# Kernel tuning notes

Hardware: AMD Instinct MI355X
Metric: run time of the kernel (lower is better)

## Reference

```python
import jax, jax.numpy as jnp
import numpy as np

WIDTH = 1024
NUM_HEADS = 16
HEAD_DIM = WIDTH // NUM_HEADS  # 64
WINDOW = 256
BATCH = 2
SEQ = 2048
_MIN_LOGITS_VALUE = -1e30


def setup_inputs() -> dict:
    key = jax.random.key(0)
    ks = jax.random.split(key, 6)
    std = 1.0 / np.sqrt(WIDTH)
    x = jax.random.normal(ks[0], (BATCH, SEQ, WIDTH), dtype=jnp.float32)
    Wq = jax.random.normal(ks[1], (WIDTH, WIDTH), dtype=jnp.float32) * std
    Wk = jax.random.normal(ks[2], (HEAD_DIM, WIDTH), dtype=jnp.float32) * std
    Wv = jax.random.normal(ks[3], (HEAD_DIM, WIDTH), dtype=jnp.float32) * std
    Wf = jax.random.normal(ks[4], (WIDTH, WIDTH), dtype=jnp.float32) * std  # variance_scale=1.0
    bf = jnp.zeros((WIDTH,), dtype=jnp.float32)
    return {"x": x, "Wq": Wq, "Wk": Wk, "Wv": Wv, "Wf": Wf, "bf": bf}


def reference(x, Wq, Wk, Wv, Wf, bf):
    b, t, _ = x.shape
    # projections (torch Linear: y = x @ W.T)
    q = (x @ Wq.T).reshape(b, t, NUM_HEADS, HEAD_DIM)  # b t n h
    k = x @ Wk.T  # b t h  (MQA: single shared key head)
    v = x @ Wv.T  # b t h
    scale = 1.0 / np.sqrt(HEAD_DIM)
    # logits: queries per-head against the shared key head
    logits = jnp.einsum('btnh,bsh->bnts', q, k) * scale  # b n t s
    # symmetric local window mask |i - j| <= WINDOW
    pos = jnp.arange(t)
    mask = jnp.abs(pos[:, None] - pos[None, :]) <= WINDOW  # t s
    masked = jnp.where(mask[None, None, :, :], logits, _MIN_LOGITS_VALUE)
    probs = jax.nn.softmax(masked.astype(jnp.float32), axis=-1).astype(logits.dtype)
    out = jnp.einsum('bnts,bsh->btnh', probs, v).reshape(b, t, WIDTH)
    return out @ Wf.T + bf
```

## Files before the change

kernel.cpp:

```cpp
#include <hip/hip_runtime.h>

typedef __bf16 bf16;
typedef __bf16 bf16x8 __attribute__((ext_vector_type(8)));
typedef float  f32x4  __attribute__((ext_vector_type(4)));

#define MFMA(a, b, c) __builtin_amdgcn_mfma_f32_16x16x32_bf16((a), (b), (c), 0, 0, 0)

static constexpr int B_   = 2;
static constexpr int T_   = 2048;
static constexpr int D_   = 1024;
static constexpr int NH_  = 16;
static constexpr int HD_  = 64;
static constexpr int WIN_ = 256;
static constexpr int M_   = B_ * T_;
static constexpr int NQKV = D_ + 2 * HD_;

static constexpr float QSCALE = 0.125f * 1.44269504088896f;

__device__ __forceinline__ void gld_lds16(const bf16* g, bf16* l) {
  __builtin_amdgcn_global_load_lds(
      (const __attribute__((address_space(1))) void*)g,
      (__attribute__((address_space(3))) void*)l, 16, 0, 0);
}


__global__ __launch_bounds__(256) void conv_all(
    const float* __restrict__ x,  const float* __restrict__ wq,
    const float* __restrict__ wk, const float* __restrict__ wv,
    const float* __restrict__ wf, const float* __restrict__ bv,
    bf16* __restrict__ xc, bf16* __restrict__ wqkv,
    bf16* __restrict__ wfc, bf16* __restrict__ bfc) {
  const long i = (long)(blockIdx.x * 256 + threadIdx.x) * 4;
  const float* src; bf16* dst; long off;
  if      (i < 4194304L) { src = x;  dst = xc;              off = 0; }
  else if (i < 5242880L) { src = wq; dst = wqkv;            off = 4194304L; }
  else if (i < 5308416L) { src = wk; dst = wqkv + 1048576L; off = 5242880L; }
  else if (i < 5373952L) { src = wv; dst = wqkv + 1114112L; off = 5308416L; }
  else if (i < 6422528L) { src = wf; dst = wfc;             off = 5373952L; }
  else if (i < 6423552L) { src = bv; dst = bfc;             off = 6422528L; }
  else return;
  const long j = i - off;
  const float4 v = *(const float4*)(src + j);
  bf16 o[4] = {(bf16)v.x, (bf16)v.y, (bf16)v.z, (bf16)v.w};
  *(uint2*)(dst + j) = *(const uint2*)o;
}

template <int EPI>
__global__ __launch_bounds__(256) void gemm128x128(
    const bf16* __restrict__ A, const bf16* __restrict__ Bw,
    void* __restrict__ Cout, const bf16* __restrict__ bias,
    bf16* __restrict__ kb, bf16* __restrict__ vT, int N, int K) {
  __shared__ __align__(16) bf16 As[2][128 * 64];
  __shared__ __align__(16) bf16 Bs[2][128 * 64];

  const int tid  = threadIdx.x;
  const int w    = tid >> 6;
  const int lane = tid & 63;
  const int quad = lane >> 4;
  const int l16  = lane & 15;
  const int wm   = w & 1;
  const int wn   = w >> 1;
  const int m0   = blockIdx.x * 128;
  const int n0   = blockIdx.y * 128;
  const int lrow = lane >> 3;
  const int scol = ((lane & 7) ^ lrow) * 8;
  const int rx   = (l16 & 7) * 8;

  f32x4 acc[4][4] = {};

  auto stage = [&](int buf, int k0) {
#pragma unroll
    for (int t = 0; t < 8; ++t) {
      const int inst = w * 8 + t;
      if (inst < 16) {
        gld_lds16(&A[(size_t)(m0 + inst * 8 + lrow) * K + k0 + scol],
                  &As[buf][inst * 512]);
      } else {
        const int bi = inst - 16;
        gld_lds16(&Bw[(size_t)(n0 + bi * 8 + lrow) * K + k0 + scol],
                  &Bs[buf][bi * 512]);
      }
    }
  };

  auto compute = [&](int buf) {
#pragma unroll
    for (int kk = 0; kk < 64; kk += 32) {
      const int c = (kk + quad * 8) ^ rx;
      bf16x8 a[4], b[4];
#pragma unroll
      for (int i = 0; i < 4; ++i)
        a[i] = *(const bf16x8*)&As[buf][(wm * 64 + i * 16 + l16) * 64 + c];
#pragma unroll
      for (int j = 0; j < 4; ++j)
        b[j] = *(const bf16x8*)&Bs[buf][(wn * 64 + j * 16 + l16) * 64 + c];
#pragma unroll
      for (int i = 0; i < 4; ++i)
#pragma unroll
        for (int j = 0; j < 4; ++j) acc[i][j] = MFMA(a[i], b[j], acc[i][j]);
    }
  };

  stage(0, 0);
  __syncthreads();
  int cur = 0;
  for (int k0 = 64; k0 < K; k0 += 64) {
    stage(cur ^ 1, k0);
    compute(cur);
    __syncthreads();
    cur ^= 1;
  }
  compute(cur);

#pragma unroll
  for (int i = 0; i < 4; ++i) {
#pragma unroll
    for (int j = 0; j < 4; ++j) {
      const int col     = n0 + wn * 64 + j * 16 + l16;
      const int rowbase = m0 + wm * 64 + i * 16 + quad * 4;
      if (EPI == 1) {
        if (col < D_) {
          bf16* qb = (bf16*)Cout;
#pragma unroll
          for (int r = 0; r < 4; ++r)
            qb[(size_t)(rowbase + r) * D_ + col] = (bf16)(acc[i][j][r] * QSCALE);
        } else if (col < D_ + HD_) {
#pragma unroll
          for (int r = 0; r < 4; ++r)
            kb[(size_t)(rowbase + r) * HD_ + (col - D_)] = (bf16)acc[i][j][r];
        } else {
          bf16 o[4] = {(bf16)acc[i][j][0], (bf16)acc[i][j][1],
                       (bf16)acc[i][j][2], (bf16)acc[i][j][3]};
          *(uint2*)&vT[(size_t)(col - D_ - HD_) * M_ + rowbase] = *(const uint2*)o;
        }
      } else {
        float* outp = (float*)Cout;
        const float bvv = (float)bias[col];
#pragma unroll
        for (int r = 0; r < 4; ++r)
          outp[(size_t)(rowbase + r) * D_ + col] = acc[i][j][r] + bvv;
      }
    }
  }
}

__global__ __launch_bounds__(256) void attn_win128(
    const bf16* __restrict__ q, const bf16* __restrict__ k,
    const bf16* __restrict__ vT, bf16* __restrict__ o) {
  __shared__ __align__(16) bf16 Ks[2][64 * 64];
  __shared__ __align__(16) bf16 Vt[2][64 * 64];
  __shared__ __align__(16) bf16 Ps[128 * 72];
  __shared__ float ls[4][32];

  const int tid  = threadIdx.x;
  const int w    = tid >> 6;
  const int lane = tid & 63;
  const int quad = lane >> 4;
  const int l16  = lane & 15;
  const int lrow = lane >> 3;
  const int scol = ((lane & 7) ^ lrow) * 8;
  const int rx   = (l16 & 7) * 8;

  const int t0 = blockIdx.x * 128;
  const int n  = blockIdx.y;
  const int b  = blockIdx.z;

  auto stageKV = [&](int st, int pb) {
#pragma unroll
    for (int t = 0; t < 2; ++t) {
      const int inst = w * 2 + t;
      gld_lds16(&k[((size_t)(b * T_ + st + inst * 8 + lrow)) * HD_ + scol],
                &Ks[pb][inst * 512]);
      gld_lds16(&vT[(size_t)(inst * 8 + lrow) * M_ + b * T_ + st + scol],
                &Vt[pb][inst * 512]);
    }
  };

  const int st_lo = (t0 - WIN_ > 0) ? t0 - WIN_ : 0;
  const int st_hi = (t0 + WIN_ + 64 < T_ - 64) ? t0 + WIN_ + 64 : T_ - 64;

  stageKV(st_lo, 0);
  int pb = 0;

  bf16x8 qf[2][2];
#pragma unroll
  for (int tt = 0; tt < 2; ++tt)
#pragma unroll
    for (int kq = 0; kq < 2; ++kq)
      qf[tt][kq] = *(const bf16x8*)
          &q[((size_t)(b * T_ + t0 + w * 32 + tt * 16 + l16)) * D_ +
             n * HD_ + kq * 32 + quad * 8];

  f32x4 o_acc[2][4] = {};
  float l_part[2] = {0.0f, 0.0f};

  for (int st = st_lo; st <= st_hi; st += 64) {
    __syncthreads();
    if (st + 64 <= st_hi) stageKV(st + 64, pb ^ 1);

    f32x4 sacc[4][2] = {};
#pragma unroll
    for (int kk = 0; kk < 64; kk += 32) {
      const int c = (kk + quad * 8) ^ rx;
      bf16x8 ak[4];
#pragma unroll
      for (int stile = 0; stile < 4; ++stile)
        ak[stile] = *(const bf16x8*)&Ks[pb][(stile * 16 + l16) * 64 + c];
      __builtin_amdgcn_s_setprio(1);
#pragma unroll
      for (int stile = 0; stile < 4; ++stile)
#pragma unroll
        for (int tt = 0; tt < 2; ++tt)
          sacc[stile][tt] = MFMA(ak[stile], qf[tt][kk >> 5], sacc[stile][tt]);
      __builtin_amdgcn_s_setprio(0);
    }

    const int off_t = st - t0;
    const bool need_mask =
        (off_t < w * 32 - (WIN_ - 31)) || (off_t > w * 32 + (WIN_ - 63));
    if (!need_mask) {
#pragma unroll
      for (int tt = 0; tt < 2; ++tt) {
#pragma unroll
        for (int stile = 0; stile < 4; ++stile) {
          bf16 pk[4];
          float psum = 0.0f;
#pragma unroll
          for (int r = 0; r < 4; ++r) {
            const float p =
                __builtin_amdgcn_exp2f(fminf(sacc[stile][tt][r], 43.28f));
            psum += p;
            pk[r] = (bf16)p;
          }
          l_part[tt] += psum;
          *(uint2*)&Ps[(w * 32 + tt * 16 + l16) * 72 + stile * 16 + quad * 4] =
              *(const uint2*)pk;
        }
      }
    } else {
#pragma unroll
      for (int tt = 0; tt < 2; ++tt) {
        const int t   = t0 + w * 32 + tt * 16 + l16;
        const int tlo = t0 + w * 32 + tt * 16;
#pragma unroll
        for (int stile = 0; stile < 4; ++stile) {
          const int slo = st + stile * 16;
          if (slo - (tlo + 15) > WIN_ || tlo - (slo + 15) > WIN_) {
            const uint2 z = {0u, 0u};
            *(uint2*)&Ps[(w * 32 + tt * 16 + l16) * 72 + stile * 16 + quad * 4] = z;
          } else {
            bf16 pk[4];
            float psum = 0.0f;
#pragma unroll
            for (int r = 0; r < 4; ++r) {
              const int s = slo + quad * 4 + r;
              const int d = t - s;
              const float p =
                  (d > WIN_ || d < -WIN_)
                      ? 0.0f
                      : __builtin_amdgcn_exp2f(fminf(sacc[stile][tt][r], 43.28f));
              psum += p;
              pk[r] = (bf16)p;
            }
            l_part[tt] += psum;
            *(uint2*)&Ps[(w * 32 + tt * 16 + l16) * 72 + stile * 16 + quad * 4] =
                *(const uint2*)pk;
          }
        }
      }
    }

#pragma unroll
    for (int kk = 0; kk < 64; kk += 32) {
      const int c = (kk + quad * 8) ^ rx;
      bf16x8 ap[2];
#pragma unroll
      for (int rg = 0; rg < 2; ++rg)
        ap[rg] = *(const bf16x8*)&Ps[(w * 32 + rg * 16 + l16) * 72 + kk + quad * 8];
      __builtin_amdgcn_s_setprio(1);
#pragma unroll
      for (int nt = 0; nt < 4; ++nt) {
        bf16x8 bv = *(const bf16x8*)&Vt[pb][(nt * 16 + l16) * 64 + c];
#pragma unroll
        for (int rg = 0; rg < 2; ++rg)
          o_acc[rg][nt] = MFMA(ap[rg], bv, o_acc[rg][nt]);
      }
      __builtin_amdgcn_s_setprio(0);
    }
    pb ^= 1;
  }

#pragma unroll
  for (int tt = 0; tt < 2; ++tt) {
    l_part[tt] += __shfl_xor(l_part[tt], 16);
    l_part[tt] += __shfl_xor(l_part[tt], 32);
    if (quad == 0) ls[w][tt * 16 + l16] = l_part[tt];
  }
  __syncthreads();

#pragma unroll
  for (int rg = 0; rg < 2; ++rg) {
#pragma unroll
    for (int r = 0; r < 4; ++r) {
      const float lr = ls[w][rg * 16 + quad * 4 + r] + 1e-30f;
      const int t = t0 + w * 32 + rg * 16 + quad * 4 + r;
#pragma unroll
      for (int nt = 0; nt < 4; ++nt) {
        const int h = nt * 16 + l16;
        o[((size_t)(b * T_ + t)) * D_ + n * HD_ + h] =
            (bf16)(o_acc[rg][nt][r] / lr);
      }
    }
  }
}

extern "C" void kernel_launch(void* const* d_in, const int* in_sizes, int n_in,
                              void* d_out, int out_size, void* d_ws, size_t ws_size,
                              hipStream_t stream) {
  float* out = (float*)d_out;

  bf16* xc   = (bf16*)d_ws;
  bf16* wqkv = xc   + (size_t)M_ * D_;
  bf16* wfc  = wqkv + (size_t)NQKV * D_;
  bf16* bfc  = wfc  + (size_t)D_ * D_;
  bf16* qb   = bfc  + D_;
  bf16* kb   = qb   + (size_t)M_ * D_;
  bf16* vT   = kb   + (size_t)M_ * HD_;

  dim3 blk(256);
  conv_all<<<dim3((6423552 / 4 + 255) / 256), blk, 0, stream>>>(
      (const float*)d_in[0], (const float*)d_in[1], (const float*)d_in[2],
      (const float*)d_in[3], (const float*)d_in[4], (const float*)d_in[5],
      xc, wqkv, wfc, bfc);

  gemm128x128<1><<<dim3(M_ / 128, NQKV / 128), blk, 0, stream>>>(
      xc, wqkv, (void*)qb, nullptr, kb, vT, NQKV, D_);

  attn_win128<<<dim3(T_ / 128, NH_, B_), blk, 0, stream>>>(qb, kb, vT, qb);

  gemm128x128<2><<<dim3(M_ / 128, D_ / 128), blk, 0, stream>>>(
      qb, wfc, (void*)out, bfc, nullptr, nullptr, D_, D_);
}
```

Baseline: 138.9 us.

## Skip out-of-window KV steps per wave and compute row sums via MFMA

Each wave now checks whether the current 64-key step lies entirely outside the window for its 32 query rows and skips the QK, softmax and PV work for that step. The softmax denominator is no longer summed in fp32 with shuffles and an LDS reduction; it comes from an extra MFMA of the bf16 probabilities against a ones vector, which also removes the final __syncthreads. The trade-off is that the row sum is now taken from bf16-rounded probabilities, and waves in a block may diverge in how much work they do between barriers.

```diff
diff --git a/kernel.cpp b/kernel.cpp
--- a/kernel.cpp
+++ b/kernel.cpp
@@ -150,7 +150,6 @@
   __shared__ __align__(16) bf16 Ks[2][64 * 64];
   __shared__ __align__(16) bf16 Vt[2][64 * 64];
   __shared__ __align__(16) bf16 Ps[128 * 72];
-  __shared__ float ls[4][32];
 
   const int tid  = threadIdx.x;
   const int w    = tid >> 6;
@@ -164,6 +163,7 @@
   const int t0 = blockIdx.x * 128;
   const int n  = blockIdx.y;
   const int b  = blockIdx.z;
+  const int tw = t0 + w * 32;
 
   auto stageKV = [&](int st, int pb) {
 #pragma unroll
@@ -188,122 +188,115 @@
 #pragma unroll
     for (int kq = 0; kq < 2; ++kq)
       qf[tt][kq] = *(const bf16x8*)
-          &q[((size_t)(b * T_ + t0 + w * 32 + tt * 16 + l16)) * D_ +
+          &q[((size_t)(b * T_ + tw + tt * 16 + l16)) * D_ +
              n * HD_ + kq * 32 + quad * 8];
 
+  const bf16 one_ = (bf16)1.0f;
+  const bf16x8 ones = {one_, one_, one_, one_, one_, one_, one_, one_};
+
   f32x4 o_acc[2][4] = {};
-  float l_part[2] = {0.0f, 0.0f};
+  f32x4 o_l[2] = {};
 
   for (int st = st_lo; st <= st_hi; st += 64) {
     __syncthreads();
     if (st + 64 <= st_hi) stageKV(st + 64, pb ^ 1);
 
-    f32x4 sacc[4][2] = {};
-#pragma unroll
-    for (int kk = 0; kk < 64; kk += 32) {
-      const int c = (kk + quad * 8) ^ rx;
-      bf16x8 ak[4];
-#pragma unroll
-      for (int stile = 0; stile < 4; ++stile)
-        ak[stile] = *(const bf16x8*)&Ks[pb][(stile * 16 + l16) * 64 + c];
-      __builtin_amdgcn_s_setprio(1);
-#pragma unroll
-      for (int stile = 0; stile < 4; ++stile)
-#pragma unroll
-        for (int tt = 0; tt < 2; ++tt)
-          sacc[stile][tt] = MFMA(ak[stile], qf[tt][kk >> 5], sacc[stile][tt]);
-      __builtin_amdgcn_s_setprio(0);
-    }
-
-    const int off_t = st - t0;
-    const bool need_mask =
-        (off_t < w * 32 - (WIN_ - 31)) || (off_t > w * 32 + (WIN_ - 63));
-    if (!need_mask) {
-#pragma unroll
-      for (int tt = 0; tt < 2; ++tt) {
-#pragma unroll
-        for (int stile = 0; stile < 4; ++stile) {
-          bf16 pk[4];
-          float psum = 0.0f;
-#pragma unroll
-          for (int r = 0; r < 4; ++r) {
-            const float p =
-                __builtin_amdgcn_exp2f(fminf(sacc[stile][tt][r], 43.28f));
-            psum += p;
-            pk[r] = (bf16)p;
-          }
-          l_part[tt] += psum;
-          *(uint2*)&Ps[(w * 32 + tt * 16 + l16) * 72 + stile * 16 + quad * 4] =
-              *(const uint2*)pk;
-        }
-      }
-    } else {
-#pragma unroll
-      for (int tt = 0; tt < 2; ++tt) {
-        const int t   = t0 + w * 32 + tt * 16 + l16;
-        const int tlo = t0 + w * 32 + tt * 16;
-#pragma unroll
-        for (int stile = 0; stile < 4; ++stile) {
-          const int slo = st + stile * 16;
-          if (slo - (tlo + 15) > WIN_ || tlo - (slo + 15) > WIN_) {
-            const uint2 z = {0u, 0u};
-            *(uint2*)&Ps[(w * 32 + tt * 16 + l16) * 72 + stile * 16 + quad * 4] = z;
-          } else {
+    const bool step_dead =
+        (st - (tw + 31) > WIN_) || (tw - (st + 63) > WIN_);
+    if (!step_dead) {
+      f32x4 sacc[4][2] = {};
+#pragma unroll
+      for (int kk = 0; kk < 64; kk += 32) {
+        const int c = (kk + quad * 8) ^ rx;
+        bf16x8 ak[4];
+#pragma unroll
+        for (int stile = 0; stile < 4; ++stile)
+          ak[stile] = *(const bf16x8*)&Ks[pb][(stile * 16 + l16) * 64 + c];
+        __builtin_amdgcn_s_setprio(1);
+#pragma unroll
+        for (int stile = 0; stile < 4; ++stile)
+#pragma unroll
+          for (int tt = 0; tt < 2; ++tt)
+            sacc[stile][tt] = MFMA(ak[stile], qf[tt][kk >> 5], sacc[stile][tt]);
+        __builtin_amdgcn_s_setprio(0);
+      }
+
+      const int off_t = st - t0;
+      const bool need_mask =
+          (off_t < w * 32 - (WIN_ - 31)) || (off_t > w * 32 + (WIN_ - 63));
+      if (!need_mask) {
+#pragma unroll
+        for (int tt = 0; tt < 2; ++tt) {
+#pragma unroll
+          for (int stile = 0; stile < 4; ++stile) {
             bf16 pk[4];
-            float psum = 0.0f;
-#pragma unroll
-            for (int r = 0; r < 4; ++r) {
-              const int s = slo + quad * 4 + r;
-              const int d = t - s;
-              const float p =
-                  (d > WIN_ || d < -WIN_)
-                      ? 0.0f
-                      : __builtin_amdgcn_exp2f(fminf(sacc[stile][tt][r], 43.28f));
-              psum += p;
-              pk[r] = (bf16)p;
-            }
-            l_part[tt] += psum;
+#pragma unroll
+            for (int r = 0; r < 4; ++r)
+              pk[r] = (bf16)__builtin_amdgcn_exp2f(
+                  fminf(sacc[stile][tt][r], 43.28f));
             *(uint2*)&Ps[(w * 32 + tt * 16 + l16) * 72 + stile * 16 + quad * 4] =
                 *(const uint2*)pk;
           }
         }
-      }
-    }
-
-#pragma unroll
-    for (int kk = 0; kk < 64; kk += 32) {
-      const int c = (kk + quad * 8) ^ rx;
-      bf16x8 ap[2];
-#pragma unroll
-      for (int rg = 0; rg < 2; ++rg)
-        ap[rg] = *(const bf16x8*)&Ps[(w * 32 + rg * 16 + l16) * 72 + kk + quad * 8];
-      __builtin_amdgcn_s_setprio(1);
-#pragma unroll
-      for (int nt = 0; nt < 4; ++nt) {
-        bf16x8 bv = *(const bf16x8*)&Vt[pb][(nt * 16 + l16) * 64 + c];
+      } else {
+#pragma unroll
+        for (int tt = 0; tt < 2; ++tt) {
+          const int t   = tw + tt * 16 + l16;
+          const int tlo = tw + tt * 16;
+#pragma unroll
+          for (int stile = 0; stile < 4; ++stile) {
+            const int slo = st + stile * 16;
+            if (slo - (tlo + 15) > WIN_ || tlo - (slo + 15) > WIN_) {
+              const uint2 z = {0u, 0u};
+              *(uint2*)&Ps[(w * 32 + tt * 16 + l16) * 72 + stile * 16 + quad * 4] = z;
+            } else {
+              bf16 pk[4];
+#pragma unroll
+              for (int r = 0; r < 4; ++r) {
+                const int s = slo + quad * 4 + r;
+                const int d = t - s;
+                pk[r] = (d > WIN_ || d < -WIN_)
+                            ? (bf16)0.0f
+                            : (bf16)__builtin_amdgcn_exp2f(
+                                  fminf(sacc[stile][tt][r], 43.28f));
+              }
+              *(uint2*)&Ps[(w * 32 + tt * 16 + l16) * 72 + stile * 16 + quad * 4] =
+                  *(const uint2*)pk;
+            }
+          }
+        }
+      }
+
+#pragma unroll
+      for (int kk = 0; kk < 64; kk += 32) {
+        const int c = (kk + quad * 8) ^ rx;
+        bf16x8 ap[2];
 #pragma unroll
         for (int rg = 0; rg < 2; ++rg)
-          o_acc[rg][nt] = MFMA(ap[rg], bv, o_acc[rg][nt]);
-      }
-      __builtin_amdgcn_s_setprio(0);
+          ap[rg] = *(const bf16x8*)&Ps[(w * 32 + rg * 16 + l16) * 72 + kk + quad * 8];
+        __builtin_amdgcn_s_setprio(1);
+#pragma unroll
+        for (int nt = 0; nt < 4; ++nt) {
+          bf16x8 bv = *(const bf16x8*)&Vt[pb][(nt * 16 + l16) * 64 + c];
+#pragma unroll
+          for (int rg = 0; rg < 2; ++rg)
+            o_acc[rg][nt] = MFMA(ap[rg], bv, o_acc[rg][nt]);
+        }
+#pragma unroll
+        for (int rg = 0; rg < 2; ++rg)
+          o_l[rg] = MFMA(ap[rg], ones, o_l[rg]);
+        __builtin_amdgcn_s_setprio(0);
+      }
     }
     pb ^= 1;
   }
 
 #pragma unroll
-  for (int tt = 0; tt < 2; ++tt) {
-    l_part[tt] += __shfl_xor(l_part[tt], 16);
-    l_part[tt] += __shfl_xor(l_part[tt], 32);
-    if (quad == 0) ls[w][tt * 16 + l16] = l_part[tt];
-  }
-  __syncthreads();
-
-#pragma unroll
   for (int rg = 0; rg < 2; ++rg) {
 #pragma unroll
     for (int r = 0; r < 4; ++r) {
-      const float lr = ls[w][rg * 16 + quad * 4 + r] + 1e-30f;
-      const int t = t0 + w * 32 + rg * 16 + quad * 4 + r;
+      const float lr = o_l[rg][r] + 1e-30f;
+      const int t = tw + rg * 16 + quad * 4 + r;
 #pragma unroll
       for (int nt = 0; nt < 4; ++nt) {
         const int h = nt * 16 + l16;
```

Measured after the change: 139.0 us. About the same (+0.1%).
